# Kernel optimization log

Measured on AMD Instinct MI355X. Metric: run time of the kernel, lower is better.

Reference implementation:

```python
import jax, jax.numpy as jnp
import numpy as np

B, N, E, C = 8, 4096, 1024, 512


def setup_inputs() -> dict:
    key = jax.random.key(0)
    k1, k2, k3, k4 = jax.random.split(key, 4)
    node_feats = jax.random.normal(k1, (B, N, C), dtype=jnp.float32)
    hyper_feats = jax.random.normal(k2, (B, E, C), dtype=jnp.float32)
    # torch nn.Linear params: weight [out, in], bias [out]
    Wq = jax.random.normal(k3, (C, C), dtype=jnp.float32) * (1.0 / np.sqrt(C))
    bq = jnp.zeros((C,), dtype=jnp.float32)
    Wkv = jax.random.normal(k4, (2 * C, C), dtype=jnp.float32) * (1.0 / np.sqrt(C))
    bkv = jnp.zeros((2 * C,), dtype=jnp.float32)
    return {"node_feats": node_feats, "hyper_feats": hyper_feats,
            "Wq": Wq, "bq": bq, "Wkv": Wkv, "bkv": bkv}


def reference(node_feats, hyper_feats, Wq, bq, Wkv, bkv):
    C_ = node_feats.shape[-1]
    scale = C_ ** -0.5
    Q = node_feats @ Wq.T + bq                      # [B,N,C]
    KV = hyper_feats @ Wkv.T + bkv                  # [B,E,2C]
    K, V = KV[..., :C_], KV[..., C_:]               # [B,E,C] each
    attn = jnp.einsum('bnc,bec->bne', Q, K) * scale  # [B,N,E]
    attn = jax.nn.softmax(attn, axis=-1)
    return jnp.einsum('bne,bec->bnc', attn, V)       # [B,N,C]
```

## Files before the change

### kernel.cpp

```cpp
#include <hip/hip_runtime.h>
#include <cstdint>
#include <cstddef>

typedef _Float16 h16;
typedef _Float16 h16x4 __attribute__((ext_vector_type(4)));
typedef _Float16 h16x8 __attribute__((ext_vector_type(8)));
typedef float fx4 __attribute__((ext_vector_type(4)));

static constexpr int B_ = 8, N_ = 4096, E_ = 1024, C_ = 512;
static constexpr float SCALE = 0.044194173824159216f;

__device__ __forceinline__ void glds16(const h16* g, h16* l) {
  __builtin_amdgcn_global_load_lds(
      (const __attribute__((address_space(1))) unsigned int*)g,
      (__attribute__((address_space(3))) unsigned int*)l, 16, 0, 0);
}

__global__ __launch_bounds__(256) void cvt_kernel(const float* __restrict__ src,
                                                  h16* __restrict__ dst, int n8) {
  int i = blockIdx.x * 256 + threadIdx.x;
  if (i >= n8) return;
  const float4* s4 = (const float4*)src;
  float4 a = s4[2 * i], b = s4[2 * i + 1];
  h16x8 o;
  o[0] = (h16)a.x; o[1] = (h16)a.y; o[2] = (h16)a.z; o[3] = (h16)a.w;
  o[4] = (h16)b.x; o[5] = (h16)b.y; o[6] = (h16)b.z; o[7] = (h16)b.w;
  *(h16x8*)(dst + (size_t)i * 8) = o;
}

template <int MODE>
__global__ __launch_bounds__(512, 4) void gemm128(
    const h16* __restrict__ A, const h16* __restrict__ Bm,
    const float* __restrict__ bias,
    h16* __restrict__ outH, h16* __restrict__ outK, h16* __restrict__ outVt,
    float* __restrict__ outF, float* __restrict__ rowsum,
    int Ncols, int K) {
  extern __shared__ h16 lds[];
  const int tid = threadIdx.x;
  const int wave = tid >> 6, lane = tid & 63;
  const int wm = wave >> 2, wn = wave & 3;
  const int lr = lane & 15, kq = lane >> 4;
  const int mBase = blockIdx.x * 128, nBase = blockIdx.y * 256;
  const int z = blockIdx.z;
  if (MODE == 2) { A += (size_t)z * N_ * C_; Bm += (size_t)z * E_ * C_;
                   outH += (size_t)z * N_ * E_; rowsum += (size_t)z * N_; }
  if (MODE == 3) { A += (size_t)z * N_ * E_; Bm += (size_t)z * C_ * E_;
                   outF += (size_t)z * N_ * C_; rowsum += (size_t)z * N_; }

  fx4 acc[4][4];
#pragma unroll
  for (int i = 0; i < 4; ++i)
#pragma unroll
    for (int j = 0; j < 4; ++j) acc[i][j] = (fx4){0.f, 0.f, 0.f, 0.f};

  int aoff[4], boff[4];
#pragma unroll
  for (int f = 0; f < 4; ++f) {
    int row = wm * 64 + f * 16 + lr;
    int r2 = row >> 1;
    int s8 = (((row & 1) << 2) | kq) ^ (r2 & 7);
    aoff[f] = r2 * 64 + s8 * 8;
  }
#pragma unroll
  for (int n = 0; n < 4; ++n) {
    int row = wn * 64 + n * 16 + lr;
    int r2 = row >> 1;
    int s8 = (((row & 1) << 2) | kq) ^ (r2 & 7);
    boff[n] = 4096 + r2 * 64 + s8 * 8;
  }

  unsigned aS, bS[2];
  {
    int r2 = tid >> 3;
    int so8 = (tid & 7) ^ (r2 & 7);
    aS = (unsigned)((mBase + 2 * r2 + (so8 >> 2)) * K + (so8 & 3) * 8);
  }
#pragma unroll
  for (int i = 0; i < 2; ++i) {
    int r2 = i * 64 + (tid >> 3);
    int so8 = (tid & 7) ^ (r2 & 7);
    bS[i] = (unsigned)((nBase + 2 * r2 + (so8 >> 2)) * K + (so8 & 3) * 8);
  }
  const int KH = K >> 5;

  auto stage = [&](int kh, int si) {
    h16* slot = lds + si * 12288;
    int kc = kh * 32;
    glds16(A + aS + kc, slot + wave * 512);
    glds16(Bm + bS[0] + kc, slot + 4096 + wave * 512);
    glds16(Bm + bS[1] + kc, slot + 8192 + wave * 512);
  };

  stage(0, 0);
  stage(1, 1);
  asm volatile("s_waitcnt vmcnt(3)" ::: "memory");
  __builtin_amdgcn_s_barrier();

  int siR = 0, siS = 2;
  for (int kh = 0; kh < KH; ++kh) {
    const int sb = siR * 12288;
    h16x8 af[4], bf[4];
#pragma unroll
    for (int i = 0; i < 4; ++i) af[i] = *(const h16x8*)&lds[sb + aoff[i]];
#pragma unroll
    for (int i = 0; i < 4; ++i) bf[i] = *(const h16x8*)&lds[sb + boff[i]];
    if (kh + 2 < KH) stage(kh + 2, siS);
    if (kh < KH - 2) {
      asm volatile("s_waitcnt vmcnt(3)" ::: "memory");
    } else {
      asm volatile("s_waitcnt vmcnt(0)" ::: "memory");
    }
    __builtin_amdgcn_s_barrier();
    asm volatile("s_waitcnt lgkmcnt(0)" ::: "memory");
    __builtin_amdgcn_sched_barrier(0);
    __builtin_amdgcn_s_setprio(1);
#pragma unroll
    for (int mi = 0; mi < 4; ++mi)
#pragma unroll
      for (int ni = 0; ni < 4; ++ni)
        acc[mi][ni] = __builtin_amdgcn_mfma_f32_16x16x32_f16(af[mi], bf[ni],
                                                             acc[mi][ni], 0, 0, 0);
    __builtin_amdgcn_s_setprio(0);
    __builtin_amdgcn_s_barrier();
    siR = (siR == 2) ? 0 : siR + 1;
    siS = (siS == 2) ? 0 : siS + 1;
  }

  const int rbase = kq * 4;
  if (MODE == 2) {
#pragma unroll
    for (int mi = 0; mi < 4; ++mi) {
#pragma unroll
      for (int r = 0; r < 4; ++r) {
        int row = mBase + wm * 64 + mi * 16 + rbase + r;
        float rs = 0.f;
#pragma unroll
        for (int ni = 0; ni < 4; ++ni) {
          int col = nBase + wn * 64 + ni * 16 + lr;
          float e = __expf(acc[mi][ni][r] * SCALE);
          rs += e;
          outH[(size_t)row * Ncols + col] = (h16)e;
        }
        rs += __shfl_xor(rs, 1); rs += __shfl_xor(rs, 2);
        rs += __shfl_xor(rs, 4); rs += __shfl_xor(rs, 8);
        if (lr == 0) atomicAdd(&rowsum[row], rs);
      }
    }
  } else if (MODE == 3) {
#pragma unroll
    for (int mi = 0; mi < 4; ++mi) {
#pragma unroll
      for (int r = 0; r < 4; ++r) {
        int row = mBase + wm * 64 + mi * 16 + rbase + r;
        float inv = 1.0f / rowsum[row];
#pragma unroll
        for (int ni = 0; ni < 4; ++ni) {
          int col = nBase + wn * 64 + ni * 16 + lr;
          outF[(size_t)row * Ncols + col] = acc[mi][ni][r] * inv;
        }
      }
    }
  } else {
    float bv[4];
#pragma unroll
    for (int ni = 0; ni < 4; ++ni) bv[ni] = bias[nBase + wn * 64 + ni * 16 + lr];
#pragma unroll
    for (int mi = 0; mi < 4; ++mi) {
      int row0 = mBase + wm * 64 + mi * 16 + rbase;
#pragma unroll
      for (int ni = 0; ni < 4; ++ni) {
        int col = nBase + wn * 64 + ni * 16 + lr;
        if (MODE == 1 && col >= C_) {
          h16x4 pk;
#pragma unroll
          for (int r = 0; r < 4; ++r) pk[r] = (h16)(acc[mi][ni][r] + bv[ni]);
          int zb = row0 >> 10, e = row0 & 1023;
          *(h16x4*)&outVt[((size_t)zb * C_ + (col - C_)) * E_ + e] = pk;
        } else {
#pragma unroll
          for (int r = 0; r < 4; ++r) {
            float v = acc[mi][ni][r] + bv[ni];
            if (MODE == 0) outH[(size_t)(row0 + r) * Ncols + col] = (h16)v;
            else           outK[(size_t)(row0 + r) * C_ + col] = (h16)v;
          }
        }
      }
    }
  }
}

extern "C" void kernel_launch(void* const* d_in, const int* in_sizes, int n_in,
                              void* d_out, int out_size, void* d_ws, size_t ws_size,
                              hipStream_t stream) {
  const float* node  = (const float*)d_in[0];
  const float* hyper = (const float*)d_in[1];
  const float* Wq    = (const float*)d_in[2];
  const float* bq    = (const float*)d_in[3];
  const float* Wkv   = (const float*)d_in[4];
  const float* bkv   = (const float*)d_in[5];
  float* out = (float*)d_out;
  char* ws = (char*)d_ws;

  h16* S_h     = (h16*)(ws + 0);
  h16* node_h  = (h16*)(ws + 0);
  h16* hyper_h = (h16*)(ws + 33554432);
  h16* Q_h     = (h16*)(ws + 67108864);
  h16* K_h     = (h16*)(ws + 100663296);
  h16* Vt_h    = (h16*)(ws + 109051904);
  h16* Wq_h    = (h16*)(ws + 117440512);
  h16* Wkv_h   = (h16*)(ws + 117964800);
  float* rowsum = (float*)(ws + 119013376);
  if (ws_size < 119144448u) return;

  static int attr_done = 0;
  if (!attr_done) {
    hipFuncSetAttribute(reinterpret_cast<const void*>(&gemm128<0>),
                        hipFuncAttributeMaxDynamicSharedMemorySize, 73728);
    hipFuncSetAttribute(reinterpret_cast<const void*>(&gemm128<1>),
                        hipFuncAttributeMaxDynamicSharedMemorySize, 73728);
    hipFuncSetAttribute(reinterpret_cast<const void*>(&gemm128<2>),
                        hipFuncAttributeMaxDynamicSharedMemorySize, 73728);
    hipFuncSetAttribute(reinterpret_cast<const void*>(&gemm128<3>),
                        hipFuncAttributeMaxDynamicSharedMemorySize, 73728);
    attr_done = 1;
  }

  cvt_kernel<<<dim3(C_ * C_ / 8 / 256), 256, 0, stream>>>(Wq, Wq_h, C_ * C_ / 8);
  cvt_kernel<<<dim3(2 * C_ * C_ / 8 / 256), 256, 0, stream>>>(Wkv, Wkv_h, 2 * C_ * C_ / 8);
  cvt_kernel<<<dim3(B_ * N_ * C_ / 8 / 256), 256, 0, stream>>>(node, node_h, B_ * N_ * C_ / 8);
  cvt_kernel<<<dim3(B_ * E_ * C_ / 8 / 256), 256, 0, stream>>>(hyper, hyper_h, B_ * E_ * C_ / 8);
  hipMemsetAsync(rowsum, 0, (size_t)B_ * N_ * sizeof(float), stream);

  gemm128<0><<<dim3(B_ * N_ / 128, C_ / 256), 512, 73728, stream>>>(
      node_h, Wq_h, bq, Q_h, nullptr, nullptr, nullptr, nullptr, C_, C_);
  gemm128<1><<<dim3(B_ * E_ / 128, 2 * C_ / 256), 512, 73728, stream>>>(
      hyper_h, Wkv_h, bkv, nullptr, K_h, Vt_h, nullptr, nullptr, 2 * C_, C_);
  gemm128<2><<<dim3(N_ / 128, E_ / 256, B_), 512, 73728, stream>>>(
      Q_h, K_h, nullptr, S_h, nullptr, nullptr, nullptr, rowsum, E_, C_);
  gemm128<3><<<dim3(N_ / 128, C_ / 256, B_), 512, 73728, stream>>>(
      S_h, Vt_h, nullptr, nullptr, nullptr, nullptr, out, rowsum, C_, E_);
}
```

Baseline: 272.2 us.

## Fuse QK^T, softmax and PV into a single flash-attention style kernel

Replaces the separate score GEMM (which wrote an fp16 [B,N,E] exp matrix plus atomic rowsums) and the PV GEMM with one fused kernel. Each block keeps 64 query rows in LDS and streams K and V tiles directly from global memory. Exponentiated scores are staged through LDS, and row sums are reduced on chip. This removes the large intermediate score round trip through HBM and the memset/atomic rowsum pass. In exchange, K/V loads are not staged through shared memory, the block uses 96KB of LDS with lower occupancy, and there is no max-subtraction, just as before.

```diff
diff --git a/kernel.cpp b/kernel.cpp
--- a/kernel.cpp
+++ b/kernel.cpp
@@ -33,7 +33,6 @@
     const h16* __restrict__ A, const h16* __restrict__ Bm,
     const float* __restrict__ bias,
     h16* __restrict__ outH, h16* __restrict__ outK, h16* __restrict__ outVt,
-    float* __restrict__ outF, float* __restrict__ rowsum,
     int Ncols, int K) {
   extern __shared__ h16 lds[];
   const int tid = threadIdx.x;
@@ -41,11 +40,6 @@
   const int wm = wave >> 2, wn = wave & 3;
   const int lr = lane & 15, kq = lane >> 4;
   const int mBase = blockIdx.x * 128, nBase = blockIdx.y * 256;
-  const int z = blockIdx.z;
-  if (MODE == 2) { A += (size_t)z * N_ * C_; Bm += (size_t)z * E_ * C_;
-                   outH += (size_t)z * N_ * E_; rowsum += (size_t)z * N_; }
-  if (MODE == 3) { A += (size_t)z * N_ * E_; Bm += (size_t)z * C_ * E_;
-                   outF += (size_t)z * N_ * C_; rowsum += (size_t)z * N_; }
 
   fx4 acc[4][4];
 #pragma unroll
@@ -127,66 +121,152 @@
   }
 
   const int rbase = kq * 4;
-  if (MODE == 2) {
-#pragma unroll
-    for (int mi = 0; mi < 4; ++mi) {
-#pragma unroll
-      for (int r = 0; r < 4; ++r) {
-        int row = mBase + wm * 64 + mi * 16 + rbase + r;
-        float rs = 0.f;
-#pragma unroll
-        for (int ni = 0; ni < 4; ++ni) {
-          int col = nBase + wn * 64 + ni * 16 + lr;
-          float e = __expf(acc[mi][ni][r] * SCALE);
-          rs += e;
-          outH[(size_t)row * Ncols + col] = (h16)e;
-        }
-        rs += __shfl_xor(rs, 1); rs += __shfl_xor(rs, 2);
-        rs += __shfl_xor(rs, 4); rs += __shfl_xor(rs, 8);
-        if (lr == 0) atomicAdd(&rowsum[row], rs);
-      }
-    }
-  } else if (MODE == 3) {
-#pragma unroll
-    for (int mi = 0; mi < 4; ++mi) {
-#pragma unroll
-      for (int r = 0; r < 4; ++r) {
-        int row = mBase + wm * 64 + mi * 16 + rbase + r;
-        float inv = 1.0f / rowsum[row];
-#pragma unroll
-        for (int ni = 0; ni < 4; ++ni) {
-          int col = nBase + wn * 64 + ni * 16 + lr;
-          outF[(size_t)row * Ncols + col] = acc[mi][ni][r] * inv;
+  float bv[4];
+#pragma unroll
+  for (int ni = 0; ni < 4; ++ni) bv[ni] = bias[nBase + wn * 64 + ni * 16 + lr];
+#pragma unroll
+  for (int mi = 0; mi < 4; ++mi) {
+    int row0 = mBase + wm * 64 + mi * 16 + rbase;
+#pragma unroll
+    for (int ni = 0; ni < 4; ++ni) {
+      int col = nBase + wn * 64 + ni * 16 + lr;
+      if (MODE == 1 && col >= C_) {
+        h16x4 pk;
+#pragma unroll
+        for (int r = 0; r < 4; ++r) pk[r] = (h16)(acc[mi][ni][r] + bv[ni]);
+        int zb = row0 >> 10, e = row0 & 1023;
+        *(h16x4*)&outVt[((size_t)zb * C_ + (col - C_)) * E_ + e] = pk;
+      } else {
+#pragma unroll
+        for (int r = 0; r < 4; ++r) {
+          float v = acc[mi][ni][r] + bv[ni];
+          if (MODE == 0) outH[(size_t)(row0 + r) * Ncols + col] = (h16)v;
+          else           outK[(size_t)(row0 + r) * C_ + col] = (h16)v;
         }
       }
     }
-  } else {
-    float bv[4];
-#pragma unroll
-    for (int ni = 0; ni < 4; ++ni) bv[ni] = bias[nBase + wn * 64 + ni * 16 + lr];
-#pragma unroll
-    for (int mi = 0; mi < 4; ++mi) {
-      int row0 = mBase + wm * 64 + mi * 16 + rbase;
-#pragma unroll
-      for (int ni = 0; ni < 4; ++ni) {
-        int col = nBase + wn * 64 + ni * 16 + lr;
-        if (MODE == 1 && col >= C_) {
-          h16x4 pk;
-#pragma unroll
-          for (int r = 0; r < 4; ++r) pk[r] = (h16)(acc[mi][ni][r] + bv[ni]);
-          int zb = row0 >> 10, e = row0 & 1023;
-          *(h16x4*)&outVt[((size_t)zb * C_ + (col - C_)) * E_ + e] = pk;
-        } else {
-#pragma unroll
-          for (int r = 0; r < 4; ++r) {
-            float v = acc[mi][ni][r] + bv[ni];
-            if (MODE == 0) outH[(size_t)(row0 + r) * Ncols + col] = (h16)v;
-            else           outK[(size_t)(row0 + r) * C_ + col] = (h16)v;
-          }
+  }
+}
+
+__global__ __launch_bounds__(512) void fa_kernel(
+    const h16* __restrict__ Q, const h16* __restrict__ K,
+    const h16* __restrict__ Vt, float* __restrict__ out) {
+  extern __shared__ h16 lds[];
+  const int id = blockIdx.x;
+  const int z = id & 7, qt = id >> 3;
+  const h16* Qz = Q + ((size_t)z * N_ + (size_t)qt * 64) * C_;
+  const h16* Kz = K + (size_t)z * E_ * C_;
+  const h16* Vz = Vt + (size_t)z * C_ * E_;
+  float* Oz = out + ((size_t)z * N_ + (size_t)qt * 64) * C_;
+  const int tid = threadIdx.x, wave = tid >> 6, lane = tid & 63;
+  const int lr = lane & 15, kq = lane >> 4;
+
+#pragma unroll
+  for (int i = 0; i < 8; ++i) {
+    int g = i * 512 + tid;
+    int st = g >> 8, idx = g & 255;
+    int r2 = idx >> 3, so8 = (idx & 7) ^ (r2 & 7);
+    glds16(Qz + (size_t)(2 * r2 + (so8 >> 2)) * C_ + st * 32 + (so8 & 3) * 8,
+           lds + g * 8);
+  }
+
+  const h16* kp0 = Kz + (size_t)(wave * 32 + lr) * C_ + kq * 8;
+  const h16* kp1 = kp0 + (size_t)16 * C_;
+  const h16* vp[4];
+#pragma unroll
+  for (int ni = 0; ni < 4; ++ni)
+    vp[ni] = Vz + (size_t)(wave * 64 + ni * 16 + lr) * E_ + kq * 8;
+
+  const int s8q = (((lr & 1) << 2) | kq) ^ ((lr >> 1) & 7);
+  const int qb = (lr >> 1) * 64 + s8q * 8;
+
+  fx4 o[4][4];
+#pragma unroll
+  for (int i = 0; i < 4; ++i)
+#pragma unroll
+    for (int j = 0; j < 4; ++j) o[i][j] = (fx4){0.f, 0.f, 0.f, 0.f};
+  float rs[4][4] = {{0.f}};
+
+  __syncthreads();
+
+  for (int ec = 0; ec < 4; ++ec) {
+    fx4 s[4][2];
+#pragma unroll
+    for (int i = 0; i < 4; ++i) { s[i][0] = (fx4){0.f,0.f,0.f,0.f};
+                                  s[i][1] = (fx4){0.f,0.f,0.f,0.f}; }
+#pragma unroll
+    for (int kh = 0; kh < 16; ++kh) {
+      h16x8 kb0 = *(const h16x8*)(kp0 + kh * 32);
+      h16x8 kb1 = *(const h16x8*)(kp1 + kh * 32);
+      h16x8 qa[4];
+#pragma unroll
+      for (int mi = 0; mi < 4; ++mi)
+        qa[mi] = *(const h16x8*)&lds[kh * 2048 + mi * 512 + qb];
+#pragma unroll
+      for (int mi = 0; mi < 4; ++mi) {
+        s[mi][0] = __builtin_amdgcn_mfma_f32_16x16x32_f16(qa[mi], kb0, s[mi][0], 0, 0, 0);
+        s[mi][1] = __builtin_amdgcn_mfma_f32_16x16x32_f16(qa[mi], kb1, s[mi][1], 0, 0, 0);
+      }
+    }
+    __syncthreads();
+#pragma unroll
+    for (int mi = 0; mi < 4; ++mi)
+#pragma unroll
+      for (int r = 0; r < 4; ++r) {
+        int rb = kq * 2 + (r >> 1);
+        int roff = 32768 + wave * 2048 + (mi * 8 + rb) * 64;
+#pragma unroll
+        for (int ni = 0; ni < 2; ++ni) {
+          float e = __expf(s[mi][ni][r] * SCALE);
+          rs[mi][r] += e;
+          int s8p = (((r & 1) << 2) | (ni * 2 + (lr >> 3))) ^ (rb & 7);
+          lds[roff + s8p * 8 + (lr & 7)] = (h16)e;
         }
       }
-    }
-  }
+    __syncthreads();
+#pragma unroll
+    for (int vs = 0; vs < 8; ++vs) {
+      h16x8 vb[4], pa[4];
+#pragma unroll
+      for (int ni = 0; ni < 4; ++ni)
+        vb[ni] = *(const h16x8*)(vp[ni] + ec * 256 + vs * 32);
+#pragma unroll
+      for (int mi = 0; mi < 4; ++mi)
+        pa[mi] = *(const h16x8*)&lds[32768 + vs * 2048 + mi * 512 + qb];
+#pragma unroll
+      for (int mi = 0; mi < 4; ++mi)
+#pragma unroll
+        for (int ni = 0; ni < 4; ++ni)
+          o[mi][ni] = __builtin_amdgcn_mfma_f32_16x16x32_f16(pa[mi], vb[ni], o[mi][ni], 0, 0, 0);
+    }
+    kp0 += (size_t)256 * C_;
+    kp1 += (size_t)256 * C_;
+  }
+
+  __syncthreads();
+  float* rsl = (float*)&lds[32768];
+  if (tid < 64) rsl[tid] = 0.f;
+  __syncthreads();
+#pragma unroll
+  for (int mi = 0; mi < 4; ++mi)
+#pragma unroll
+    for (int r = 0; r < 4; ++r) {
+      float v = rs[mi][r];
+      v += __shfl_xor(v, 1); v += __shfl_xor(v, 2);
+      v += __shfl_xor(v, 4); v += __shfl_xor(v, 8);
+      if (lr == 0) atomicAdd(&rsl[mi * 16 + kq * 4 + r], v);
+    }
+  __syncthreads();
+#pragma unroll
+  for (int mi = 0; mi < 4; ++mi)
+#pragma unroll
+    for (int r = 0; r < 4; ++r) {
+      int row = mi * 16 + kq * 4 + r;
+      float inv = 1.0f / rsl[row];
+#pragma unroll
+      for (int ni = 0; ni < 4; ++ni)
+        Oz[(size_t)row * C_ + wave * 64 + ni * 16 + lr] = o[mi][ni][r] * inv;
+    }
 }
 
 extern "C" void kernel_launch(void* const* d_in, const int* in_sizes, int n_in,
@@ -201,7 +281,6 @@
   float* out = (float*)d_out;
   char* ws = (char*)d_ws;
 
-  h16* S_h     = (h16*)(ws + 0);
   h16* node_h  = (h16*)(ws + 0);
   h16* hyper_h = (h16*)(ws + 33554432);
   h16* Q_h     = (h16*)(ws + 67108864);
@@ -209,8 +288,7 @@
   h16* Vt_h    = (h16*)(ws + 109051904);
   h16* Wq_h    = (h16*)(ws + 117440512);
   h16* Wkv_h   = (h16*)(ws + 117964800);
-  float* rowsum = (float*)(ws + 119013376);
-  if (ws_size < 119144448u) return;
+  if (ws_size < 119013376u) return;
 
   static int attr_done = 0;
   if (!attr_done) {
@@ -218,10 +296,8 @@
                         hipFuncAttributeMaxDynamicSharedMemorySize, 73728);
     hipFuncSetAttribute(reinterpret_cast<const void*>(&gemm128<1>),
                         hipFuncAttributeMaxDynamicSharedMemorySize, 73728);
-    hipFuncSetAttribute(reinterpret_cast<const void*>(&gemm128<2>),
-                        hipFuncAttributeMaxDynamicSharedMemorySize, 73728);
-    hipFuncSetAttribute(reinterpret_cast<const void*>(&gemm128<3>),
-                        hipFuncAttributeMaxDynamicSharedMemorySize, 73728);
+    hipFuncSetAttribute(reinterpret_cast<const void*>(&fa_kernel),
+                        hipFuncAttributeMaxDynamicSharedMemorySize, 98304);
     attr_done = 1;
   }
 
@@ -229,14 +305,10 @@
   cvt_kernel<<<dim3(2 * C_ * C_ / 8 / 256), 256, 0, stream>>>(Wkv, Wkv_h, 2 * C_ * C_ / 8);
   cvt_kernel<<<dim3(B_ * N_ * C_ / 8 / 256), 256, 0, stream>>>(node, node_h, B_ * N_ * C_ / 8);
   cvt_kernel<<<dim3(B_ * E_ * C_ / 8 / 256), 256, 0, stream>>>(hyper, hyper_h, B_ * E_ * C_ / 8);
-  hipMemsetAsync(rowsum, 0, (size_t)B_ * N_ * sizeof(float), stream);
 
   gemm128<0><<<dim3(B_ * N_ / 128, C_ / 256), 512, 73728, stream>>>(
-      node_h, Wq_h, bq, Q_h, nullptr, nullptr, nullptr, nullptr, C_, C_);
+      node_h, Wq_h, bq, Q_h, nullptr, nullptr, C_, C_);
   gemm128<1><<<dim3(B_ * E_ / 128, 2 * C_ / 256), 512, 73728, stream>>>(
-      hyper_h, Wkv_h, bkv, nullptr, K_h, Vt_h, nullptr, nullptr, 2 * C_, C_);
-  gemm128<2><<<dim3(N_ / 128, E_ / 256, B_), 512, 73728, stream>>>(
-      Q_h, K_h, nullptr, S_h, nullptr, nullptr, nullptr, rowsum, E_, C_);
-  gemm128<3><<<dim3(N_ / 128, C_ / 256, B_), 512, 73728, stream>>>(
-      S_h, Vt_h, nullptr, nullptr, nullptr, nullptr, out, rowsum, C_, E_);
-}
+      hyper_h, Wkv_h, bkv, nullptr, K_h, Vt_h, 2 * C_, C_);
+  fa_kernel<<<dim3(B_ * N_ / 64), 512, 98304, stream>>>(Q_h, K_h, Vt_h, out);
+}
```

After: 330.3 us. 21.3% more time.
